# Kernel optimization log

Hardware: AMD Instinct MI355X
Metric: run time of the kernel (lower is better)

## Reference

```python
import jax, jax.numpy as jnp
import numpy as np

IDIM = 1024
ODIM = 1024
NHEADS = 16
B, S = 4, 1024


def setup_inputs() -> dict:
    key = jax.random.key(0)
    k1, k2, k3, k4, k5, k6 = jax.random.split(key, 6)
    m_feats = jax.random.normal(k1, (B, S, IDIM), dtype=jnp.float32)
    mask = jax.random.randint(k2, (B, S), 0, 2, dtype=jnp.int32)
    # torch Linear weights stored pre-transposed: y = x @ W + b
    W_c = jax.random.normal(k3, (IDIM, 2 * ODIM), dtype=jnp.float32) * 0.02
    b_c = jnp.zeros((2 * ODIM,), dtype=jnp.float32)
    W_v = jax.random.normal(k4, (IDIM, ODIM), dtype=jnp.float32) * 0.02
    b_v = jnp.zeros((ODIM,), dtype=jnp.float32)
    return {"m_feats": m_feats, "mask": mask, "W_c": W_c, "b_c": b_c, "W_v": W_v, "b_v": b_v}


def reference(m_feats, mask, W_c, b_c, W_v, b_v):
    # dp = 0.0 -> dropout is identity (eval-mode equivalence)
    Bn, Sn, _ = m_feats.shape
    odim = W_v.shape[1]
    dh = odim // NHEADS
    m_k = m_feats @ W_v + b_v            # v_lin  -> keys   [B,S,odim]
    m_trans = m_feats @ W_c + b_c        # c_lin  -> [B,S,2*odim]
    m_q = m_trans[..., :odim]            # queries
    m_v = m_trans[..., odim:]            # values
    mk = m_k.reshape(Bn, Sn, NHEADS, dh)
    mq = m_q.reshape(Bn, Sn, NHEADS, dh)
    mv = m_v.reshape(Bn, Sn, NHEADS, dh)
    # original: scores = K @ Q^T / sqrt(dh); softmax over the Q (last) axis
    scores = jnp.einsum('bihd,bjhd->bhij', mk, mq) / jnp.sqrt(jnp.float32(dh))
    maskf = mask.astype(jnp.float32)
    scores = jnp.where(maskf[:, None, None, :] == 0.0, jnp.float32(-1e9), scores)
    w = jax.nn.softmax(scores, axis=-1)               # [B,H,S,S]
    r = jnp.einsum('bhij,bjhd->bihd', w, mv).reshape(Bn, Sn, odim)
    updated_m = m_feats + r
    return updated_m, w
```

## Files before the change

kernel.cpp:

```cpp
#include <hip/hip_runtime.h>
#include <cstddef>

typedef short short8 __attribute__((ext_vector_type(8)));
typedef float f32x4 __attribute__((ext_vector_type(4)));

#define SS 1024
#define NH 16
#define DH 64
#define NB 4

static __device__ __forceinline__ unsigned short f2bf(float f) {
    union { float f; unsigned int i; } x; x.f = f;
    unsigned int r = x.i + 0x7FFFu + ((x.i >> 16) & 1u);
    return (unsigned short)(r >> 16);
}
static __device__ __forceinline__ float bf2f(unsigned short u) {
    union { unsigned int i; float f; } x; x.i = ((unsigned int)u) << 16;
    return x.f;
}

static __device__ __forceinline__ void g2l16(const void* g, void* l) {
    __builtin_amdgcn_global_load_lds(
        (const __attribute__((address_space(1))) unsigned int*)g,
        (__attribute__((address_space(3))) unsigned int*)l, 16, 0, 0);
}

__global__ __launch_bounds__(256) void prep(const float* __restrict__ mf,
                                            unsigned short* __restrict__ mfb,
                                            const float* __restrict__ Wv,
                                            const float* __restrict__ Wc,
                                            unsigned short* __restrict__ WT) {
    __shared__ float tile[32][33];
    int bx = blockIdx.x;
    int t = threadIdx.x;
    if (bx < 2048) {
        size_t i = ((size_t)bx * 256 + t) * 8;
        float4 v0 = *(const float4*)(mf + i);
        float4 v1 = *(const float4*)(mf + i + 4);
        short8 o;
        o[0] = (short)f2bf(v0.x); o[1] = (short)f2bf(v0.y);
        o[2] = (short)f2bf(v0.z); o[3] = (short)f2bf(v0.w);
        o[4] = (short)f2bf(v1.x); o[5] = (short)f2bf(v1.y);
        o[6] = (short)f2bf(v1.z); o[7] = (short)f2bf(v1.w);
        *(short8*)(mfb + i) = o;
        return;
    }
    bx -= 2048;
    int n0 = (bx % 96) * 32, k0 = (bx / 96) * 32;
    int kr = t >> 3, nc = (t & 7) * 4;
    const float* src; int ld; int nn = n0 + nc;
    if (n0 < 1024) { src = Wv; ld = 1024; } else { src = Wc; ld = 2048; nn -= 1024; }
    float4 v = *(const float4*)(src + (size_t)(k0 + kr) * ld + nn);
    tile[kr][nc + 0] = v.x; tile[kr][nc + 1] = v.y;
    tile[kr][nc + 2] = v.z; tile[kr][nc + 3] = v.w;
    __syncthreads();
    int nr = t >> 3, kc = (t & 7) * 4;
    short4 o;
    o.x = (short)f2bf(tile[kc + 0][nr]); o.y = (short)f2bf(tile[kc + 1][nr]);
    o.z = (short)f2bf(tile[kc + 2][nr]); o.w = (short)f2bf(tile[kc + 3][nr]);
    *(short4*)(WT + (size_t)(n0 + nr) * 1024 + k0 + kc) = o;
}

__global__ __launch_bounds__(256) void gemm_kqv(const unsigned short* __restrict__ A,
                                                const unsigned short* __restrict__ BT,
                                                const float* __restrict__ bv,
                                                const float* __restrict__ bc,
                                                unsigned short* __restrict__ kq,
                                                unsigned short* __restrict__ mvT) {
    __shared__ __align__(16) unsigned short As[2][128 * 32];
    __shared__ __align__(16) unsigned short Bs[2][128 * 32];
    int lin = blockIdx.y * 24 + blockIdx.x;
    int xcd = lin & 7, idx = lin >> 3;
    int cx = xcd & 1, cy = xcd >> 1;
    int xi = idx % 12, yi = idx / 12;
    int n0 = (cx * 12 + xi) * 128;
    int m0 = (cy * 8 + yi) * 128;

    int tid = threadIdx.x, lane = tid & 63, wv = tid >> 6;
    int wm = wv >> 1, wn = wv & 1;
    int lq = lane & 15, quad = lane >> 4;

    f32x4 zero = {0.f, 0.f, 0.f, 0.f};
    f32x4 acc[4][4];
#pragma unroll
    for (int i = 0; i < 4; ++i)
#pragma unroll
        for (int j = 0; j < 4; ++j) acc[i][j] = zero;

    int r0 = tid >> 2, s0 = tid & 3;
    int c0 = s0 ^ ((r0 >> 1) & 3);
    int r1 = (tid + 256) >> 2, s1 = tid & 3;
    int c1 = s1 ^ ((r1 >> 1) & 3);

    const unsigned short* Abase0 = A + (size_t)(m0 + r0) * 1024 + c0 * 8;
    const unsigned short* Abase1 = A + (size_t)(m0 + r1) * 1024 + c1 * 8;
    const unsigned short* Bbase0 = BT + (size_t)(n0 + r0) * 1024 + c0 * 8;
    const unsigned short* Bbase1 = BT + (size_t)(n0 + r1) * 1024 + c1 * 8;

    g2l16(Abase0, As[0] + tid * 8);
    g2l16(Abase1, As[0] + (tid + 256) * 8);
    g2l16(Bbase0, Bs[0] + tid * 8);
    g2l16(Bbase1, Bs[0] + (tid + 256) * 8);
    __syncthreads();

#pragma unroll 2
    for (int t32 = 0; t32 < 32; ++t32) {
        int cur = t32 & 1;
        if (t32 < 31) {
            int nkt = (t32 + 1) * 32;
            g2l16(Abase0 + nkt, As[cur ^ 1] + tid * 8);
            g2l16(Abase1 + nkt, As[cur ^ 1] + (tid + 256) * 8);
            g2l16(Bbase0 + nkt, Bs[cur ^ 1] + tid * 8);
            g2l16(Bbase1 + nkt, Bs[cur ^ 1] + (tid + 256) * 8);
        }

        short8 af[4], bfr[4];
#pragma unroll
        for (int i = 0; i < 4; ++i) {
            int Ra = wm * 64 + i * 16 + lq;
            af[i] = *(const short8*)(As[cur] + Ra * 32 + (quad ^ ((Ra >> 1) & 3)) * 8);
            int Rb = wn * 64 + i * 16 + lq;
            bfr[i] = *(const short8*)(Bs[cur] + Rb * 32 + (quad ^ ((Rb >> 1) & 3)) * 8);
        }
#pragma unroll
        for (int mi = 0; mi < 4; ++mi)
#pragma unroll
            for (int ni = 0; ni < 4; ++ni)
                acc[mi][ni] = __builtin_amdgcn_mfma_f32_16x16x32_bf16(af[mi], bfr[ni], acc[mi][ni], 0, 0, 0);

        __syncthreads();
    }

#pragma unroll
    for (int mi = 0; mi < 4; ++mi) {
#pragma unroll
        for (int ni = 0; ni < 4; ++ni) {
            int colg = n0 + wn * 64 + ni * 16 + lq;
            float bias = (colg < 1024) ? bv[colg] : bc[colg - 1024];
            if (colg < 2048) {
#pragma unroll
                for (int r = 0; r < 4; ++r) {
                    int rowg = m0 + wm * 64 + mi * 16 + quad * 4 + r;
                    kq[(size_t)rowg * 2048 + colg] = f2bf(acc[mi][ni][r] + bias);
                }
            } else {
                int c = colg - 2048;
                int hh = c >> 6, dd = c & 63;
#pragma unroll
                for (int r = 0; r < 4; ++r) {
                    int rowg = m0 + wm * 64 + mi * 16 + quad * 4 + r;
                    int bb = rowg >> 10, jj = rowg & 1023;
                    mvT[((size_t)(bb * NH + hh) * DH + dd) * 1024 + jj] =
                        f2bf(acc[mi][ni][r] + bias);
                }
            }
        }
    }
}

__global__ __launch_bounds__(256, 4) void attn_kernel(const unsigned short* __restrict__ kq,
                                                      const unsigned short* __restrict__ mvT,
                                                      const int* __restrict__ mask,
                                                      const float* __restrict__ m_feats,
                                                      float* __restrict__ out0,
                                                      float* __restrict__ out1) {
    __shared__ __align__(16) unsigned short mk_s[16 * 72];
    __shared__ __align__(16) unsigned short s_exp[16 * 1032];
    __shared__ float wsum[4][16];
    __shared__ float inv_s[16];

    int tid = threadIdx.x;
    int lane = tid & 63, wv = tid >> 6;
    int lq = lane & 15, quad = lane >> 4;

    int blk = ((int)blockIdx.x & 7) * 512 + ((int)blockIdx.x >> 3);
    int it = blk & 63;
    int bh = blk >> 6;
    int h = bh & (NH - 1), b = bh >> 4;
    int i0 = it * 16;

    const float SC = 0.18033688011112042f;
    const unsigned short* mqb = kq + (size_t)b * SS * 2048 + 1024 + h * 64 + quad * 8;
    const int* maskb = mask + (size_t)b * SS;

    short8 qb[2][4][2];
    int qm[2][4];
    float sums[4] = {0.f, 0.f, 0.f, 0.f};

#define QLOAD(p, s)                                                          \
    {                                                                        \
        int jb_ = (s) * 256 + wv * 64;                                       \
        _Pragma("unroll") for (int js = 0; js < 4; ++js) {                   \
            int jg_ = jb_ + js * 16 + lq;                                    \
            size_t ro_ = (size_t)jg_ * 2048;                                 \
            qb[p][js][0] = *(const short8*)(mqb + ro_);                      \
            qb[p][js][1] = *(const short8*)(mqb + ro_ + 32);                 \
            qm[p][js] = maskb[jg_];                                          \
        }                                                                    \
    }

#define QCOMP(p, s)                                                          \
    {                                                                        \
        int jb_ = (s) * 256 + wv * 64;                                       \
        _Pragma("unroll") for (int js = 0; js < 4; ++js) {                   \
            f32x4 acc = {0.f, 0.f, 0.f, 0.f};                                \
            acc = __builtin_amdgcn_mfma_f32_16x16x32_bf16(a0, qb[p][js][0], acc, 0, 0, 0); \
            acc = __builtin_amdgcn_mfma_f32_16x16x32_bf16(a1, qb[p][js][1], acc, 0, 0, 0); \
            int jc_ = jb_ + js * 16 + lq;                                    \
            _Pragma("unroll") for (int r = 0; r < 4; ++r) {                  \
                float e = qm[p][js] ? __builtin_amdgcn_exp2f(acc[r] * SC) : 0.f; \
                sums[r] += e;                                                \
                s_exp[(quad * 4 + r) * 1032 + jc_] = f2bf(e);                \
            }                                                                \
        }                                                                    \
    }

    QLOAD(0, 0);

    float mf4[4];
#pragma unroll
    for (int r = 0; r < 4; ++r) {
        size_t o = (size_t)(b * SS + i0 + quad * 4 + r) * 1024 + h * 64 + wv * 16 + lq;
        mf4[r] = m_feats[o];
    }

    if (tid < 128) {
        int row = tid >> 3, ch = tid & 7;
        int4 v = *(const int4*)(kq + (size_t)(b * SS + i0 + row) * 2048 + h * 64 + ch * 8);
        *(int4*)(mk_s + row * 72 + ch * 8) = v;
    }
    QLOAD(1, 1);
    __syncthreads();

    short8 a0 = *(const short8*)(mk_s + lq * 72 + 0 * 32 + quad * 8);
    short8 a1 = *(const short8*)(mk_s + lq * 72 + 1 * 32 + quad * 8);

    QCOMP(0, 0); QLOAD(0, 2);
    QCOMP(1, 1); QLOAD(1, 3);
    QCOMP(0, 2);
    QCOMP(1, 3);
#undef QLOAD
#undef QCOMP

    f32x4 racc = {0.f, 0.f, 0.f, 0.f};
    const unsigned short* mvb = mvT + ((size_t)bh * DH + wv * 16 + lq) * 1024 + quad * 8;
    size_t wbase = ((size_t)bh * SS + i0) * SS;
    short8 vbuf[4][4];

#define VLOAD(p, ko)                                                         \
    {                                                                        \
        _Pragma("unroll") for (int k2 = 0; k2 < 4; ++k2)                     \
            vbuf[p][k2] = *(const short8*)(mvb + ((ko) * 4 + k2) * 32);      \
    }

#define VCOMP(p, ko)                                                         \
    {                                                                        \
        _Pragma("unroll") for (int k2 = 0; k2 < 4; ++k2) {                   \
            short8 ae = *(const short8*)(s_exp + lq * 1032 + ((ko) * 4 + k2) * 32 + quad * 8); \
            racc = __builtin_amdgcn_mfma_f32_16x16x32_bf16(ae, vbuf[p][k2], racc, 0, 0, 0); \
        }                                                                    \
    }

#define WOUT(r)                                                              \
    {                                                                        \
        float iv = inv_s[r];                                                 \
        short4 ev = *(const short4*)(s_exp + (r) * 1032 + tid * 4);          \
        f32x4 wo;                                                            \
        wo[0] = bf2f((unsigned short)ev.x) * iv;                             \
        wo[1] = bf2f((unsigned short)ev.y) * iv;                             \
        wo[2] = bf2f((unsigned short)ev.z) * iv;                             \
        wo[3] = bf2f((unsigned short)ev.w) * iv;                             \
        __builtin_nontemporal_store(wo, (f32x4*)(out1 + wbase + (size_t)(r) * SS + tid * 4)); \
    }

    VLOAD(0, 0); VLOAD(1, 1);

#pragma unroll
    for (int r = 0; r < 4; ++r) {
        float s = sums[r];
        s += __shfl_xor(s, 1); s += __shfl_xor(s, 2);
        s += __shfl_xor(s, 4); s += __shfl_xor(s, 8);
        if (lq == 0) wsum[wv][quad * 4 + r] = s;
    }
    __syncthreads();
    if (tid < 16) {
        float s = wsum[0][tid] + wsum[1][tid] + wsum[2][tid] + wsum[3][tid];
        inv_s[tid] = 1.0f / s;
    }
    VLOAD(2, 2); VLOAD(3, 3);
    __syncthreads();

    VCOMP(0, 0); VLOAD(0, 4); WOUT(0);  WOUT(1);
    VCOMP(1, 1); VLOAD(1, 5); WOUT(2);  WOUT(3);
    VCOMP(2, 2); VLOAD(2, 6); WOUT(4);  WOUT(5);
    VCOMP(3, 3); VLOAD(3, 7); WOUT(6);  WOUT(7);
    VCOMP(0, 4); WOUT(8);  WOUT(9);
    VCOMP(1, 5); WOUT(10); WOUT(11);
    VCOMP(2, 6); WOUT(12); WOUT(13);
    VCOMP(3, 7); WOUT(14); WOUT(15);
#undef VLOAD
#undef VCOMP
#undef WOUT

#pragma unroll
    for (int r = 0; r < 4; ++r) {
        int row = quad * 4 + r;
        size_t o = (size_t)(b * SS + i0 + row) * 1024 + h * 64 + wv * 16 + lq;
        __builtin_nontemporal_store(mf4[r] + racc[r] * inv_s[row], out0 + o);
    }
}

extern "C" void kernel_launch(void* const* d_in, const int* in_sizes, int n_in,
                              void* d_out, int out_size, void* d_ws, size_t ws_size,
                              hipStream_t stream) {
    const float* m_feats = (const float*)d_in[0];
    const int*   mask    = (const int*)d_in[1];
    const float* W_c     = (const float*)d_in[2];
    const float* b_c     = (const float*)d_in[3];
    const float* W_v     = (const float*)d_in[4];
    const float* b_v     = (const float*)d_in[5];

    float* out0 = (float*)d_out;
    float* out1 = out0 + (size_t)NB * SS * 1024;

    unsigned short* mf_bf = (unsigned short*)d_ws;
    unsigned short* WT    = mf_bf + (size_t)4096 * 1024;
    unsigned short* kq    = WT + (size_t)3072 * 1024;
    unsigned short* mvT   = kq + (size_t)4096 * 2048;

    prep<<<dim3(5120), dim3(256), 0, stream>>>(m_feats, mf_bf, W_v, W_c, WT);
    gemm_kqv<<<dim3(24, 32), dim3(256), 0, stream>>>(mf_bf, WT, b_v, b_c, kq, mvT);
    attn_kernel<<<dim3(4096), dim3(256), 0, stream>>>(kq, mvT, mask, m_feats, out0, out1);
}
```

Before: 421.3 us.

## Process 32 query rows per attention block to reuse Q and V tiles

Each attention block now handles 32 rows of keys instead of 16, so every loaded Q and V fragment feeds two MFMA tiles. This halves the global reads of Q, V and mask per output row and halves the grid to 2048 blocks. In exchange it roughly doubles shared memory (about 66KB for s_exp) and registers per block, and drops the occupancy hint from 4 to 2 blocks per CU. Runtime is likely dominated by the large fp32 attention-weight write, which this change does not alter.

New measurement: 375.4 us (median of 2 runs). 10.9% less time.

```diff
diff --git a/kernel.cpp b/kernel.cpp
--- a/kernel.cpp
+++ b/kernel.cpp
@@ -158,26 +158,26 @@
     }
 }
 
-__global__ __launch_bounds__(256, 4) void attn_kernel(const unsigned short* __restrict__ kq,
+__global__ __launch_bounds__(256, 2) void attn_kernel(const unsigned short* __restrict__ kq,
                                                       const unsigned short* __restrict__ mvT,
                                                       const int* __restrict__ mask,
                                                       const float* __restrict__ m_feats,
                                                       float* __restrict__ out0,
                                                       float* __restrict__ out1) {
-    __shared__ __align__(16) unsigned short mk_s[16 * 72];
-    __shared__ __align__(16) unsigned short s_exp[16 * 1032];
-    __shared__ float wsum[4][16];
-    __shared__ float inv_s[16];
+    __shared__ __align__(16) unsigned short mk_s[32 * 72];
+    __shared__ __align__(16) unsigned short s_exp[32 * 1032];
+    __shared__ float wsum[4][32];
+    __shared__ float inv_s[32];
 
     int tid = threadIdx.x;
     int lane = tid & 63, wv = tid >> 6;
     int lq = lane & 15, quad = lane >> 4;
 
-    int blk = ((int)blockIdx.x & 7) * 512 + ((int)blockIdx.x >> 3);
-    int it = blk & 63;
-    int bh = blk >> 6;
+    int blk = ((int)blockIdx.x & 7) * 256 + ((int)blockIdx.x >> 3);
+    int it = blk & 31;
+    int bh = blk >> 5;
     int h = bh & (NH - 1), b = bh >> 4;
-    int i0 = it * 16;
+    int i0 = it * 32;
 
     const float SC = 0.18033688011112042f;
     const unsigned short* mqb = kq + (size_t)b * SS * 2048 + 1024 + h * 64 + quad * 8;
@@ -185,7 +185,7 @@
 
     short8 qb[2][4][2];
     int qm[2][4];
-    float sums[4] = {0.f, 0.f, 0.f, 0.f};
+    float sums[2][4] = {{0.f, 0.f, 0.f, 0.f}, {0.f, 0.f, 0.f, 0.f}};
 
 #define QLOAD(p, s)                                                          \
     {                                                                        \
@@ -203,28 +203,32 @@
     {                                                                        \
         int jb_ = (s) * 256 + wv * 64;                                       \
         _Pragma("unroll") for (int js = 0; js < 4; ++js) {                   \
-            f32x4 acc = {0.f, 0.f, 0.f, 0.f};                                \
-            acc = __builtin_amdgcn_mfma_f32_16x16x32_bf16(a0, qb[p][js][0], acc, 0, 0, 0); \
-            acc = __builtin_amdgcn_mfma_f32_16x16x32_bf16(a1, qb[p][js][1], acc, 0, 0, 0); \
             int jc_ = jb_ + js * 16 + lq;                                    \
-            _Pragma("unroll") for (int r = 0; r < 4; ++r) {                  \
-                float e = qm[p][js] ? __builtin_amdgcn_exp2f(acc[r] * SC) : 0.f; \
-                sums[r] += e;                                                \
-                s_exp[(quad * 4 + r) * 1032 + jc_] = f2bf(e);                \
+            _Pragma("unroll") for (int ti = 0; ti < 2; ++ti) {               \
+                f32x4 acc = {0.f, 0.f, 0.f, 0.f};                            \
+                acc = __builtin_amdgcn_mfma_f32_16x16x32_bf16(a[ti][0], qb[p][js][0], acc, 0, 0, 0); \
+                acc = __builtin_amdgcn_mfma_f32_16x16x32_bf16(a[ti][1], qb[p][js][1], acc, 0, 0, 0); \
+                _Pragma("unroll") for (int r = 0; r < 4; ++r) {              \
+                    float e = qm[p][js] ? __builtin_amdgcn_exp2f(acc[r] * SC) : 0.f; \
+                    sums[ti][r] += e;                                        \
+                    s_exp[(ti * 16 + quad * 4 + r) * 1032 + jc_] = f2bf(e);  \
+                }                                                            \
             }                                                                \
         }                                                                    \
     }
 
     QLOAD(0, 0);
 
-    float mf4[4];
-#pragma unroll
-    for (int r = 0; r < 4; ++r) {
-        size_t o = (size_t)(b * SS + i0 + quad * 4 + r) * 1024 + h * 64 + wv * 16 + lq;
-        mf4[r] = m_feats[o];
-    }
-
-    if (tid < 128) {
+    float mf8[2][4];
+#pragma unroll
+    for (int ti = 0; ti < 2; ++ti)
+#pragma unroll
+        for (int r = 0; r < 4; ++r) {
+            size_t o = (size_t)(b * SS + i0 + ti * 16 + quad * 4 + r) * 1024 + h * 64 + wv * 16 + lq;
+            mf8[ti][r] = m_feats[o];
+        }
+
+    {
         int row = tid >> 3, ch = tid & 7;
         int4 v = *(const int4*)(kq + (size_t)(b * SS + i0 + row) * 2048 + h * 64 + ch * 8);
         *(int4*)(mk_s + row * 72 + ch * 8) = v;
@@ -232,8 +236,12 @@
     QLOAD(1, 1);
     __syncthreads();
 
-    short8 a0 = *(const short8*)(mk_s + lq * 72 + 0 * 32 + quad * 8);
-    short8 a1 = *(const short8*)(mk_s + lq * 72 + 1 * 32 + quad * 8);
+    short8 a[2][2];
+#pragma unroll
+    for (int ti = 0; ti < 2; ++ti) {
+        a[ti][0] = *(const short8*)(mk_s + (ti * 16 + lq) * 72 + 0 * 32 + quad * 8);
+        a[ti][1] = *(const short8*)(mk_s + (ti * 16 + lq) * 72 + 1 * 32 + quad * 8);
+    }
 
     QCOMP(0, 0); QLOAD(0, 2);
     QCOMP(1, 1); QLOAD(1, 3);
@@ -242,7 +250,7 @@
 #undef QLOAD
 #undef QCOMP
 
-    f32x4 racc = {0.f, 0.f, 0.f, 0.f};
+    f32x4 racc[2] = {{0.f, 0.f, 0.f, 0.f}, {0.f, 0.f, 0.f, 0.f}};
     const unsigned short* mvb = mvT + ((size_t)bh * DH + wv * 16 + lq) * 1024 + quad * 8;
     size_t wbase = ((size_t)bh * SS + i0) * SS;
     short8 vbuf[4][4];
@@ -256,8 +264,10 @@
 #define VCOMP(p, ko)                                                         \
     {                                                                        \
         _Pragma("unroll") for (int k2 = 0; k2 < 4; ++k2) {                   \
-            short8 ae = *(const short8*)(s_exp + lq * 1032 + ((ko) * 4 + k2) * 32 + quad * 8); \
-            racc = __builtin_amdgcn_mfma_f32_16x16x32_bf16(ae, vbuf[p][k2], racc, 0, 0, 0); \
+            _Pragma("unroll") for (int ti = 0; ti < 2; ++ti) {               \
+                short8 ae = *(const short8*)(s_exp + (ti * 16 + lq) * 1032 + ((ko) * 4 + k2) * 32 + quad * 8); \
+                racc[ti] = __builtin_amdgcn_mfma_f32_16x16x32_bf16(ae, vbuf[p][k2], racc[ti], 0, 0, 0); \
+            }                                                                \
         }                                                                    \
     }
 
@@ -276,38 +286,42 @@
     VLOAD(0, 0); VLOAD(1, 1);
 
 #pragma unroll
-    for (int r = 0; r < 4; ++r) {
-        float s = sums[r];
-        s += __shfl_xor(s, 1); s += __shfl_xor(s, 2);
-        s += __shfl_xor(s, 4); s += __shfl_xor(s, 8);
-        if (lq == 0) wsum[wv][quad * 4 + r] = s;
-    }
-    __syncthreads();
-    if (tid < 16) {
+    for (int ti = 0; ti < 2; ++ti)
+#pragma unroll
+        for (int r = 0; r < 4; ++r) {
+            float s = sums[ti][r];
+            s += __shfl_xor(s, 1); s += __shfl_xor(s, 2);
+            s += __shfl_xor(s, 4); s += __shfl_xor(s, 8);
+            if (lq == 0) wsum[wv][ti * 16 + quad * 4 + r] = s;
+        }
+    __syncthreads();
+    if (tid < 32) {
         float s = wsum[0][tid] + wsum[1][tid] + wsum[2][tid] + wsum[3][tid];
         inv_s[tid] = 1.0f / s;
     }
     VLOAD(2, 2); VLOAD(3, 3);
     __syncthreads();
 
-    VCOMP(0, 0); VLOAD(0, 4); WOUT(0);  WOUT(1);
-    VCOMP(1, 1); VLOAD(1, 5); WOUT(2);  WOUT(3);
-    VCOMP(2, 2); VLOAD(2, 6); WOUT(4);  WOUT(5);
-    VCOMP(3, 3); VLOAD(3, 7); WOUT(6);  WOUT(7);
-    VCOMP(0, 4); WOUT(8);  WOUT(9);
-    VCOMP(1, 5); WOUT(10); WOUT(11);
-    VCOMP(2, 6); WOUT(12); WOUT(13);
-    VCOMP(3, 7); WOUT(14); WOUT(15);
+    VCOMP(0, 0); VLOAD(0, 4); WOUT(0);  WOUT(1);  WOUT(2);  WOUT(3);
+    VCOMP(1, 1); VLOAD(1, 5); WOUT(4);  WOUT(5);  WOUT(6);  WOUT(7);
+    VCOMP(2, 2); VLOAD(2, 6); WOUT(8);  WOUT(9);  WOUT(10); WOUT(11);
+    VCOMP(3, 3); VLOAD(3, 7); WOUT(12); WOUT(13); WOUT(14); WOUT(15);
+    VCOMP(0, 4); WOUT(16); WOUT(17); WOUT(18); WOUT(19);
+    VCOMP(1, 5); WOUT(20); WOUT(21); WOUT(22); WOUT(23);
+    VCOMP(2, 6); WOUT(24); WOUT(25); WOUT(26); WOUT(27);
+    VCOMP(3, 7); WOUT(28); WOUT(29); WOUT(30); WOUT(31);
 #undef VLOAD
 #undef VCOMP
 #undef WOUT
 
 #pragma unroll
-    for (int r = 0; r < 4; ++r) {
-        int row = quad * 4 + r;
-        size_t o = (size_t)(b * SS + i0 + row) * 1024 + h * 64 + wv * 16 + lq;
-        __builtin_nontemporal_store(mf4[r] + racc[r] * inv_s[row], out0 + o);
-    }
+    for (int ti = 0; ti < 2; ++ti)
+#pragma unroll
+        for (int r = 0; r < 4; ++r) {
+            int row = ti * 16 + quad * 4 + r;
+            size_t o = (size_t)(b * SS + i0 + row) * 1024 + h * 64 + wv * 16 + lq;
+            __builtin_nontemporal_store(mf8[ti][r] + racc[ti][r] * inv_s[row], out0 + o);
+        }
 }
 
 extern "C" void kernel_launch(void* const* d_in, const int* in_sizes, int n_in,
@@ -330,5 +344,5 @@
 
     prep<<<dim3(5120), dim3(256), 0, stream>>>(m_feats, mf_bf, W_v, W_c, WT);
     gemm_kqv<<<dim3(24, 32), dim3(256), 0, stream>>>(mf_bf, WT, b_v, b_c, kq, mvT);
-    attn_kernel<<<dim3(4096), dim3(256), 0, stream>>>(kq, mvT, mask, m_feats, out0, out1);
-}
+    attn_kernel<<<dim3(2048), dim3(256), 0, stream>>>(kq, mvT, mask, m_feats, out0, out1);
+}
```
